# Kernel tuning notes

Measured on AMD Instinct MI355X. Metric: run time of the kernel, lower is better.

Reference implementation:

```python
import jax, jax.numpy as jnp
import numpy as np

DIM = 4096
BATCH = 64
DEFAULT_LR = 0.001
DEFAULT_ALPHA = 0.01
EPS = 1e-08


def setup_inputs() -> dict:
    key = jax.random.key(0)
    k1, k2, k3 = jax.random.split(key, 3)
    weight = jax.random.normal(k1, (DIM, DIM), dtype=jnp.float32)
    input_x = jax.random.normal(k2, (BATCH, DIM), dtype=jnp.float32)
    grad = jax.random.normal(k3, (DIM, DIM), dtype=jnp.float32)
    return {"weight": weight, "input_x": input_x, "grad": grad}


def reference(weight, input_x, grad):
    # L2-normalize inputs along last dim (normalize_inputs=True)
    x = input_x / (jnp.linalg.norm(input_x, axis=-1, keepdims=True) + EPS)
    # batched outer product averaged over batch: (dim, dim)
    outer = jnp.einsum('bi,bj->ij', x, x) / x.shape[0]
    decay_matrix = jnp.eye(DIM, dtype=weight.dtype) - DEFAULT_ALPHA * outer
    # W_{t+1} = W @ (I - alpha * outer) - lr * grad
    new_weight = weight @ decay_matrix - DEFAULT_LR * grad
    return new_weight
```

## Files before the change

kernel.cpp:

```cpp
#include <hip/hip_runtime.h>
#include <math.h>

#define DIM 4096
#define BATCH 64

typedef __attribute__((ext_vector_type(8))) short short8;
typedef __attribute__((ext_vector_type(4))) float f32x4;

__device__ __forceinline__ float4 ld4(const float* p) {
    return *reinterpret_cast<const float4*>(p);
}

__device__ __forceinline__ unsigned short f2bf(float f) {
    unsigned u = __builtin_bit_cast(unsigned, f);
    u = (u + 0x7fffu + ((u >> 16) & 1u)) >> 16;
    return (unsigned short)u;
}

__global__ __launch_bounds__(256) void k_norm(const float* __restrict__ x,
                                              unsigned short* __restrict__ xb1,
                                              unsigned short* __restrict__ xb2) {
    const int b = blockIdx.x;
    const int tid = threadIdx.x;
    const float* row = x + (size_t)b * DIM;

    float ss = 0.f;
    for (int k = tid * 4; k < DIM; k += 256 * 4) {
        float4 v = ld4(row + k);
        ss += v.x * v.x + v.y * v.y + v.z * v.z + v.w * v.w;
    }
#pragma unroll
    for (int m = 32; m >= 1; m >>= 1) ss += __shfl_xor(ss, m, 64);

    __shared__ float wsum[4];
    if ((tid & 63) == 0) wsum[tid >> 6] = ss;
    __syncthreads();
    const float total = wsum[0] + wsum[1] + wsum[2] + wsum[3];
    const float scale = 1.0f / (sqrtf(total) + 1e-8f);

    const int bt = b >> 4;
    const int li = b & 15;
    const int ks = b >> 5;
    const int hi = (b & 31) >> 3;
    const int jr = b & 7;

    for (int k = tid; k < DIM; k += 256) {
        const float v = row[k] * scale;
        const unsigned short h = f2bf(v);
        const int l1 = li | (((k & 31) >> 3) << 4);
        xb1[(size_t)((((bt * 128) + (k >> 5)) * 64 + l1) << 3) + (k & 7)] = h;
        const int l2 = (k & 15) | (hi << 4);
        xb2[(size_t)(((((k >> 4) * 2) + ks) * 64 + l2) << 3) + jr] = h;
    }
}

__global__ __launch_bounds__(1024, 4) void k_fused(const float* __restrict__ W,
                                                   const float* __restrict__ G,
                                                   const unsigned short* __restrict__ xb1,
                                                   const unsigned short* __restrict__ xb2,
                                                   float* __restrict__ out) {
    __shared__ float yp[16 * 4 * 64 * 4];
    __shared__ float y2[16 * 68];

    const int tid = threadIdx.x;
    const int wv = tid >> 6;
    const int l  = tid & 63;
    const int lr = l & 15;
    const int lh = l >> 4;
    const int i0 = blockIdx.x * 16;

    f32x4 acc0 = {0.f, 0.f, 0.f, 0.f};
    f32x4 acc1 = acc0, acc2 = acc0, acc3 = acc0;

    const short8* xb1v = (const short8*)xb1;
#pragma unroll
    for (int kb8 = 0; kb8 < 8; ++kb8) {
        const int kbg = wv * 8 + kb8;
        const float* wp = W + (size_t)(i0 + lr) * DIM + kbg * 32 + lh * 8;
        const float4 wa = ld4(wp);
        const float4 wb = ld4(wp + 4);
        short8 a;
        a[0] = (short)f2bf(wa.x); a[1] = (short)f2bf(wa.y);
        a[2] = (short)f2bf(wa.z); a[3] = (short)f2bf(wa.w);
        a[4] = (short)f2bf(wb.x); a[5] = (short)f2bf(wb.y);
        a[6] = (short)f2bf(wb.z); a[7] = (short)f2bf(wb.w);
        const int bslot = kbg * 64 + l;
        acc0 = __builtin_amdgcn_mfma_f32_16x16x32_bf16(a, xb1v[bslot         ], acc0, 0, 0, 0);
        acc1 = __builtin_amdgcn_mfma_f32_16x16x32_bf16(a, xb1v[bslot + 8192  ], acc1, 0, 0, 0);
        acc2 = __builtin_amdgcn_mfma_f32_16x16x32_bf16(a, xb1v[bslot + 16384 ], acc2, 0, 0, 0);
        acc3 = __builtin_amdgcn_mfma_f32_16x16x32_bf16(a, xb1v[bslot + 24576 ], acc3, 0, 0, 0);
    }
    {
        f32x4* dst = (f32x4*)yp;
        dst[(wv * 4 + 0) * 64 + l] = acc0;
        dst[(wv * 4 + 1) * 64 + l] = acc1;
        dst[(wv * 4 + 2) * 64 + l] = acc2;
        dst[(wv * 4 + 3) * 64 + l] = acc3;
    }
    __syncthreads();

    {
        const int r  = tid >> 6;
        const int bb = tid & 63;
        const int btt = bb >> 4;
        const int lii = (bb & 15) | ((r >> 2) << 4);
        const int jq  = r & 3;
        float s = 0.f;
#pragma unroll
        for (int w = 0; w < 16; ++w) s += yp[((w * 4 + btt) * 64 + lii) * 4 + jq];
        y2[r * 68 + bb] = s;
    }
    __syncthreads();

    const float NC = -0.01f / 64.0f;
    short8 ya0, ya1;
#pragma unroll
    for (int j = 0; j < 8; ++j) {
        ya0[j] = (short)f2bf(NC * y2[lr * 68 + lh * 8 + j]);
        ya1[j] = (short)f2bf(NC * y2[lr * 68 + 32 + lh * 8 + j]);
    }

    constexpr float LRc = 0.001f;
    const short8* xb2v = (const short8*)xb2;
#pragma unroll 4
    for (int t = 0; t < 16; ++t) {
        const int jt = wv * 16 + t;
        const int bslot = jt * 2 * 64 + l;
        f32x4 d = {0.f, 0.f, 0.f, 0.f};
        d = __builtin_amdgcn_mfma_f32_16x16x32_bf16(ya0, xb2v[bslot     ], d, 0, 0, 0);
        d = __builtin_amdgcn_mfma_f32_16x16x32_bf16(ya1, xb2v[bslot + 64], d, 0, 0, 0);
        const size_t base = (size_t)(i0 + lh * 4) * DIM + jt * 16 + lr;
#pragma unroll
        for (int q = 0; q < 4; ++q) {
            const size_t idx = base + (size_t)q * DIM;
            out[idx] = W[idx] - LRc * G[idx] + d[q];
        }
    }
}

extern "C" void kernel_launch(void* const* d_in, const int* in_sizes, int n_in,
                              void* d_out, int out_size, void* d_ws, size_t ws_size,
                              hipStream_t stream) {
    const float* W = (const float*)d_in[0];
    const float* X = (const float*)d_in[1];
    const float* G = (const float*)d_in[2];
    float* out = (float*)d_out;

    unsigned short* xb1 = (unsigned short*)d_ws;
    unsigned short* xb2 = xb1 + (size_t)DIM * BATCH;

    hipLaunchKernelGGL(k_norm, dim3(BATCH), dim3(256), 0, stream, X, xb1, xb2);
    hipLaunchKernelGGL(k_fused, dim3(DIM / 16), dim3(1024), 0, stream,
                       W, G, xb1, xb2, out);
}
```

Measured before the change: 61.41 us.

## Pipeline W/G loads through LDS with async global-to-LDS triple buffering

Reworks the fused kernel to stream W (phase 1) and W/G (phase 2) through LDS using global_load_lds with a three-buffer software pipeline, explicit waitcnt and barriers. Phase 1 changes the wave work split (4 batch tiles by 4 k-groups) and uses an XOR swizzle plus truncating bf16 packing in place of rounding. Phase 2 stages the MFMA result in LDS so the epilogue does coalesced 16-byte row-contiguous loads and stores. This is meant to hide memory latency and improve coalescing, at the cost of many barriers, heavy LDS use that may cut occupancy, and slightly different bf16 rounding.

```diff
diff --git a/kernel.cpp b/kernel.cpp
--- a/kernel.cpp
+++ b/kernel.cpp
@@ -1,21 +1,36 @@
 #include <hip/hip_runtime.h>
-#include <math.h>
 
 #define DIM 4096
 #define BATCH 64
 
 typedef __attribute__((ext_vector_type(8))) short short8;
 typedef __attribute__((ext_vector_type(4))) float f32x4;
+typedef __attribute__((ext_vector_type(4))) unsigned int u32x4;
+
+typedef __attribute__((address_space(3))) unsigned int lds_u32;
+typedef const __attribute__((address_space(1))) unsigned int glb_u32;
 
 __device__ __forceinline__ float4 ld4(const float* p) {
     return *reinterpret_cast<const float4*>(p);
 }
-
+__device__ __forceinline__ void gload_lds16(const float* g, float* l) {
+    __builtin_amdgcn_global_load_lds((glb_u32*)g, (lds_u32*)l, 16, 0, 0);
+}
 __device__ __forceinline__ unsigned short f2bf(float f) {
     unsigned u = __builtin_bit_cast(unsigned, f);
     u = (u + 0x7fffu + ((u >> 16) & 1u)) >> 16;
     return (unsigned short)u;
 }
+__device__ __forceinline__ unsigned pack_bf2(float x, float y) {
+    return (__builtin_bit_cast(unsigned, x) >> 16) |
+           (__builtin_bit_cast(unsigned, y) & 0xffff0000u);
+}
+
+#define SCHED() __builtin_amdgcn_sched_barrier(0)
+#define WAITV_(N) asm volatile("s_waitcnt vmcnt(" #N ")" ::: "memory")
+#define WAITV(N) do { WAITV_(N); SCHED(); } while (0)
+#define WAITL()  do { asm volatile("s_waitcnt lgkmcnt(0)" ::: "memory"); SCHED(); } while (0)
+#define SBAR()   do { __builtin_amdgcn_s_barrier(); SCHED(); } while (0)
 
 __global__ __launch_bounds__(256) void k_norm(const float* __restrict__ x,
                                               unsigned short* __restrict__ xb1,
@@ -59,8 +74,7 @@
                                                    const unsigned short* __restrict__ xb1,
                                                    const unsigned short* __restrict__ xb2,
                                                    float* __restrict__ out) {
-    __shared__ float yp[16 * 4 * 64 * 4];
-    __shared__ float y2[16 * 68];
+    __shared__ __align__(16) float lds[29760];
 
     const int tid = threadIdx.x;
     const int wv = tid >> 6;
@@ -68,37 +82,62 @@
     const int lr = l & 15;
     const int lh = l >> 4;
     const int i0 = blockIdx.x * 16;
-
-    f32x4 acc0 = {0.f, 0.f, 0.f, 0.f};
-    f32x4 acc1 = acc0, acc2 = acc0, acc3 = acc0;
-
     const short8* xb1v = (const short8*)xb1;
-#pragma unroll
-    for (int kb8 = 0; kb8 < 8; ++kb8) {
-        const int kbg = wv * 8 + kb8;
-        const float* wp = W + (size_t)(i0 + lr) * DIM + kbg * 32 + lh * 8;
-        const float4 wa = ld4(wp);
-        const float4 wb = ld4(wp + 4);
-        short8 a;
-        a[0] = (short)f2bf(wa.x); a[1] = (short)f2bf(wa.y);
-        a[2] = (short)f2bf(wa.z); a[3] = (short)f2bf(wa.w);
-        a[4] = (short)f2bf(wb.x); a[5] = (short)f2bf(wb.y);
-        a[6] = (short)f2bf(wb.z); a[7] = (short)f2bf(wb.w);
-        const int bslot = kbg * 64 + l;
-        acc0 = __builtin_amdgcn_mfma_f32_16x16x32_bf16(a, xb1v[bslot         ], acc0, 0, 0, 0);
-        acc1 = __builtin_amdgcn_mfma_f32_16x16x32_bf16(a, xb1v[bslot + 8192  ], acc1, 0, 0, 0);
-        acc2 = __builtin_amdgcn_mfma_f32_16x16x32_bf16(a, xb1v[bslot + 16384 ], acc2, 0, 0, 0);
-        acc3 = __builtin_amdgcn_mfma_f32_16x16x32_bf16(a, xb1v[bslot + 24576 ], acc3, 0, 0, 0);
-    }
-    {
-        f32x4* dst = (f32x4*)yp;
-        dst[(wv * 4 + 0) * 64 + l] = acc0;
-        dst[(wv * 4 + 1) * 64 + l] = acc1;
-        dst[(wv * 4 + 2) * 64 + l] = acc2;
-        dst[(wv * 4 + 3) * 64 + l] = acc3;
-    }
-    __syncthreads();
-
+    const short8* xb2v = (const short8*)xb2;
+
+    const int bt = wv & 3;
+    const int kg = wv >> 2;
+    const int key  = wv & 7;
+    const int rkey = lr & 7;
+    f32x4 acc = {0.f, 0.f, 0.f, 0.f};
+    short8 fA0, fA1, fA2, fA3, fB0, fB1, fB2, fB3;
+
+#define LOADF(SS, F0_, F1_, F2_, F3_) do { \
+    const short8* p_ = xb1v + bt * 8192 + ((SS) * 16 + kg * 4) * 64 + l; \
+    F0_ = p_[0]; F1_ = p_[64]; F2_ = p_[128]; F3_ = p_[192]; SCHED(); } while (0)
+
+#define STAGE1(SS, B_) do { \
+    const float* s_ = W + (size_t)(i0 + wv) * DIM + (SS) * 512; \
+    float* d_ = lds + (B_) * 8192 + wv * 512; \
+    gload_lds16(s_ + ((l ^ key) << 2), d_); \
+    gload_lds16(s_ + ((64 + (l ^ key)) << 2), d_ + 256); SCHED(); } while (0)
+
+#define MFMA1(B_, I_, FF_) do { \
+    const int c0_ = (kg * 4 + (I_)) * 8 + lh * 2; \
+    const f32x4 a0_ = *(const f32x4*)(lds + (B_) * 8192 + lr * 512 + ((c0_ ^ rkey) << 2)); \
+    const f32x4 a1_ = *(const f32x4*)(lds + (B_) * 8192 + lr * 512 + (((c0_ + 1) ^ rkey) << 2)); \
+    u32x4 ap_; \
+    ap_[0] = pack_bf2(a0_[0], a0_[1]); ap_[1] = pack_bf2(a0_[2], a0_[3]); \
+    ap_[2] = pack_bf2(a1_[0], a1_[1]); ap_[3] = pack_bf2(a1_[2], a1_[3]); \
+    acc = __builtin_amdgcn_mfma_f32_16x16x32_bf16(__builtin_bit_cast(short8, ap_), FF_, acc, 0, 0, 0); \
+  } while (0)
+
+#define P1_MFMA(B_, F0_, F1_, F2_, F3_) do { \
+    MFMA1(B_, 0, F0_); MFMA1(B_, 1, F1_); MFMA1(B_, 2, F2_); MFMA1(B_, 3, F3_); } while (0)
+
+#define P1_STEP(SS_, NW_, BC_, BN_, FC0,FC1,FC2,FC3, FN0,FN1,FN2,FN3) do { \
+    WAITV(NW_); SBAR(); \
+    LOADF((SS_) + 1, FN0, FN1, FN2, FN3); \
+    STAGE1((SS_) + 2, BN_); \
+    P1_MFMA(BC_, FC0, FC1, FC2, FC3); } while (0)
+
+    LOADF(0, fA0, fA1, fA2, fA3);
+    STAGE1(0, 0);
+    STAGE1(1, 1);
+    P1_STEP(0, 2, 0, 2, fA0,fA1,fA2,fA3, fB0,fB1,fB2,fB3);
+    P1_STEP(1, 6, 1, 0, fB0,fB1,fB2,fB3, fA0,fA1,fA2,fA3);
+    P1_STEP(2, 6, 2, 1, fA0,fA1,fA2,fA3, fB0,fB1,fB2,fB3);
+    P1_STEP(3, 6, 0, 2, fB0,fB1,fB2,fB3, fA0,fA1,fA2,fA3);
+    P1_STEP(4, 6, 1, 0, fA0,fA1,fA2,fA3, fB0,fB1,fB2,fB3);
+    P1_STEP(5, 6, 2, 1, fB0,fB1,fB2,fB3, fA0,fA1,fA2,fA3);
+    WAITV(6); SBAR();
+    LOADF(7, fB0, fB1, fB2, fB3);
+    P1_MFMA(0, fA0, fA1, fA2, fA3);
+    WAITV(4); SBAR();
+    P1_MFMA(1, fB0, fB1, fB2, fB3);
+
+    ((f32x4*)(lds + 24576))[wv * 64 + l] = acc;
+    __syncthreads();
     {
         const int r  = tid >> 6;
         const int bb = tid & 63;
@@ -107,8 +146,9 @@
         const int jq  = r & 3;
         float s = 0.f;
 #pragma unroll
-        for (int w = 0; w < 16; ++w) s += yp[((w * 4 + btt) * 64 + lii) * 4 + jq];
-        y2[r * 68 + bb] = s;
+        for (int g = 0; g < 4; ++g)
+            s += lds[24576 + ((g * 4 + btt) * 64 + lii) * 4 + jq];
+        lds[28672 + r * 68 + bb] = s;
     }
     __syncthreads();
 
@@ -116,26 +156,77 @@
     short8 ya0, ya1;
 #pragma unroll
     for (int j = 0; j < 8; ++j) {
-        ya0[j] = (short)f2bf(NC * y2[lr * 68 + lh * 8 + j]);
-        ya1[j] = (short)f2bf(NC * y2[lr * 68 + 32 + lh * 8 + j]);
-    }
+        ya0[j] = (short)f2bf(NC * lds[28672 + lr * 68 + lh * 8 + j]);
+        ya1[j] = (short)f2bf(NC * lds[28672 + lr * 68 + 32 + lh * 8 + j]);
+    }
+    __syncthreads();
 
     constexpr float LRc = 0.001f;
-    const short8* xb2v = (const short8*)xb2;
-#pragma unroll 4
-    for (int t = 0; t < 16; ++t) {
-        const int jt = wv * 16 + t;
-        const int bslot = jt * 2 * 64 + l;
-        f32x4 d = {0.f, 0.f, 0.f, 0.f};
-        d = __builtin_amdgcn_mfma_f32_16x16x32_bf16(ya0, xb2v[bslot     ], d, 0, 0, 0);
-        d = __builtin_amdgcn_mfma_f32_16x16x32_bf16(ya1, xb2v[bslot + 64], d, 0, 0, 0);
-        const size_t base = (size_t)(i0 + lh * 4) * DIM + jt * 16 + lr;
-#pragma unroll
-        for (int q = 0; q < 4; ++q) {
-            const size_t idx = base + (size_t)q * DIM;
-            out[idx] = W[idx] - LRc * G[idx] + d[q];
-        }
-    }
+    short8 xA0, xA1, xB0, xB1;
+
+#define LOADX(C_, X0_, X1_) do { \
+    const short8* p_ = xb2v + ((C_) * 16 + wv) * 128 + l; \
+    X0_ = p_[0]; X1_ = p_[64]; SCHED(); } while (0)
+
+#define STAGE2(C_, B_) do { \
+    const size_t rb_ = (size_t)(i0 + wv) * DIM + (C_) * 256 + (l << 2); \
+    gload_lds16(W + rb_, lds + (B_) * 8192 + wv * 256); \
+    gload_lds16(G + rb_, lds + (B_) * 8192 + 4096 + wv * 256); SCHED(); } while (0)
+
+#define P2_MFMA(X0_, X1_) do { \
+    f32x4 d_ = {0.f, 0.f, 0.f, 0.f}; \
+    d_ = __builtin_amdgcn_mfma_f32_16x16x32_bf16(ya0, X0_, d_, 0, 0, 0); \
+    d_ = __builtin_amdgcn_mfma_f32_16x16x32_bf16(ya1, X1_, d_, 0, 0, 0); \
+    lds[24576 + (lh * 4 + 0) * 260 + wv * 16 + lr] = d_[0]; \
+    lds[24576 + (lh * 4 + 1) * 260 + wv * 16 + lr] = d_[1]; \
+    lds[24576 + (lh * 4 + 2) * 260 + wv * 16 + lr] = d_[2]; \
+    lds[24576 + (lh * 4 + 3) * 260 + wv * 16 + lr] = d_[3]; } while (0)
+
+#define P2_EPI(C_, B_) do { \
+    const f32x4 w_ = *(const f32x4*)(lds + (B_) * 8192 + wv * 256 + (l << 2)); \
+    const f32x4 g_ = *(const f32x4*)(lds + (B_) * 8192 + 4096 + wv * 256 + (l << 2)); \
+    const f32x4 dd_ = *(const f32x4*)(lds + 24576 + wv * 260 + (l << 2)); \
+    f32x4 o_; \
+    o_[0] = w_[0] - LRc * g_[0] + dd_[0]; \
+    o_[1] = w_[1] - LRc * g_[1] + dd_[1]; \
+    o_[2] = w_[2] - LRc * g_[2] + dd_[2]; \
+    o_[3] = w_[3] - LRc * g_[3] + dd_[3]; \
+    *(f32x4*)(out + (size_t)(i0 + wv) * DIM + (C_) * 256 + (l << 2)) = o_; } while (0)
+
+#define P2_STEP(C_, NW_, BC_, BN_, XC0_, XC1_, XN0_, XN1_) do { \
+    WAITV(NW_); SBAR(); \
+    LOADX((C_) + 1, XN0_, XN1_); \
+    STAGE2((C_) + 2, BN_); \
+    P2_MFMA(XC0_, XC1_); \
+    WAITL(); SBAR(); \
+    P2_EPI(C_, BC_); } while (0)
+
+    LOADX(0, xA0, xA1);
+    STAGE2(0, 0);
+    STAGE2(1, 1);
+    P2_STEP(0,  2, 0, 2, xA0, xA1, xB0, xB1);
+    P2_STEP(1,  4, 1, 0, xB0, xB1, xA0, xA1);
+    P2_STEP(2,  4, 2, 1, xA0, xA1, xB0, xB1);
+    P2_STEP(3,  4, 0, 2, xB0, xB1, xA0, xA1);
+    P2_STEP(4,  4, 1, 0, xA0, xA1, xB0, xB1);
+    P2_STEP(5,  4, 2, 1, xB0, xB1, xA0, xA1);
+    P2_STEP(6,  4, 0, 2, xA0, xA1, xB0, xB1);
+    P2_STEP(7,  4, 1, 0, xB0, xB1, xA0, xA1);
+    P2_STEP(8,  4, 2, 1, xA0, xA1, xB0, xB1);
+    P2_STEP(9,  4, 0, 2, xB0, xB1, xA0, xA1);
+    P2_STEP(10, 4, 1, 0, xA0, xA1, xB0, xB1);
+    P2_STEP(11, 4, 2, 1, xB0, xB1, xA0, xA1);
+    P2_STEP(12, 4, 0, 2, xA0, xA1, xB0, xB1);
+    P2_STEP(13, 4, 1, 0, xB0, xB1, xA0, xA1);
+    WAITV(4); SBAR();
+    LOADX(15, xB0, xB1);
+    P2_MFMA(xA0, xA1);
+    WAITL(); SBAR();
+    P2_EPI(14, 2);
+    WAITV(2); SBAR();
+    P2_MFMA(xB0, xB1);
+    WAITL(); SBAR();
+    P2_EPI(15, 0);
 }
 
 extern "C" void kernel_launch(void* const* d_in, const int* in_sizes, int n_in,
```

Result: faster. 59.98 us (-2.3%).
